# Performance work log

Hardware: AMD Instinct MI355X
Metric: run time of the kernel (lower is better)

## Reference

```python
import jax, jax.numpy as jnp
import numpy as np

ALPHA_MAX = 0.1


def setup_inputs() -> dict:
    key = jax.random.key(0)
    ks = jax.random.split(key, 9)
    B, M, L = 256, 3, 100000
    A, H = 4096, 512
    return {
        "x": jax.random.uniform(ks[0], (B, M, L), dtype=jnp.float32),  # log1p scores, non-negative
        "active_idx": jax.random.randint(ks[1], (A,), 0, L, dtype=jnp.int64 if jax.config.jax_enable_x64 else jnp.int32),
        "global_logits": jnp.log(jnp.full((M,), 1.0 / M, dtype=jnp.float32) + 1e-12),
        "delta_w": 0.01 * jax.random.normal(ks[2], (M, L), dtype=jnp.float32),
        "bias": 0.01 * jax.random.normal(ks[3], (L,), dtype=jnp.float32),
        "log_alpha": jnp.float32(-3.0),
        "hidden_w": jax.random.normal(ks[4], (H, M * A), dtype=jnp.float32) * (1.0 / np.sqrt(M * A)),
        "hidden_b": 0.01 * jax.random.normal(ks[5], (H,), dtype=jnp.float32),
        "delta_layer_w": jax.random.normal(ks[6], (A, H), dtype=jnp.float32) * (1.0 / np.sqrt(H)),
        "delta_layer_b": 0.01 * jax.random.normal(ks[7], (A,), dtype=jnp.float32),
    }


def reference(x, active_idx, global_logits, delta_w, bias, log_alpha,
              hidden_w, hidden_b, delta_layer_w, delta_layer_b):
    B = x.shape[0]
    # base logits: elementwise weighted sum over the 3 models, per-label weights
    w_eff = jax.nn.softmax(global_logits)[:, None] + delta_w          # (M, L)
    logits = jnp.einsum("bml,ml->bl", x, w_eff) + bias                # (B, L)
    # gather active labels -> 2-layer MLP (dropout is identity in eval)
    x_active = x[:, :, active_idx].reshape(B, -1)                     # (B, M*A)
    h = jax.nn.relu(x_active @ hidden_w.T + hidden_b)                 # (B, H)
    delta_active = h @ delta_layer_w.T + delta_layer_b                # (B, A)
    # scaled scatter-add back into full logits (duplicates accumulate)
    alpha = ALPHA_MAX * jax.nn.sigmoid(log_alpha)
    logits = logits.at[:, active_idx].add(alpha * delta_active)
    return logits
```

## Files before the change

kernel.cpp:

```cpp
#include <hip/hip_runtime.h>
#include <math.h>

#define B_ 256
#define M_ 3
#define L_ 100000
#define A_ 4096
#define H_ 512
#define MA_ (M_*A_)
#define K1_ MA_
#define NZ_ 16
#define KC1_ (K1_/NZ_)
#define BCHUNK_ 4

#define NWIN_    98
#define NB_LGX_  98
#define NB_LG_   (NB_LGX_*(B_/BCHUNK_))
#define NB_HW_   3072
#define NB_W2_   1024

typedef __attribute__((ext_vector_type(8))) short bf16x8;
typedef __attribute__((ext_vector_type(8))) unsigned short u16x8;
typedef __attribute__((ext_vector_type(4))) float f32x4;
typedef __attribute__((ext_vector_type(4))) int i32x4;

static __device__ __forceinline__ f32x4 ld4(const float* p) {
    return *reinterpret_cast<const f32x4*>(p);
}
static __device__ __forceinline__ f32x4 ld4nt(const float* p) {
    return __builtin_nontemporal_load(reinterpret_cast<const f32x4*>(p));
}
static __device__ __forceinline__ void st4nt(float* p, f32x4 v) {
    __builtin_nontemporal_store(v, reinterpret_cast<f32x4*>(p));
}
static __device__ __forceinline__ unsigned short f2bf(float f) {
    unsigned u = __float_as_uint(f);
    unsigned r = (u + 0x7FFFu + ((u >> 16) & 1u)) >> 16;
    return (unsigned short)r;
}

__global__ void init_head(int* __restrict__ head) {
    int i = blockIdx.x * blockDim.x + threadIdx.x;
    if (i < L_ / 4) {
        i32x4 m1 = {-1, -1, -1, -1};
        *reinterpret_cast<i32x4*>(head + i * 4) = m1;
    }
}

__global__ void window_hist(const int* __restrict__ idx, int* __restrict__ jbase) {
    __shared__ int cnt[NWIN_];
    for (int w = threadIdx.x; w < NWIN_; w += 256) cnt[w] = 0;
    __syncthreads();
    for (int a = threadIdx.x; a < A_; a += 256) atomicAdd(&cnt[idx[a] >> 10], 1);
    __syncthreads();
    if (threadIdx.x == 0) {
        int s = 0;
        for (int w = 0; w < NWIN_; ++w) { jbase[w] = s; s += cnt[w]; }
        jbase[NWIN_] = s;
    }
}

__global__ void build_perm(const int* __restrict__ idx, const int* __restrict__ jbase,
                           int* __restrict__ a_of_j, int* __restrict__ l_of_j,
                           int* __restrict__ head2) {
    __shared__ int ml[A_];
    __shared__ int ma[A_];
    __shared__ int nm_sh;
    int w = blockIdx.x, tid = threadIdx.x;
    if (tid == 0) nm_sh = 0;
    __syncthreads();
    for (int a = tid; a < A_; a += 256) {
        int l = idx[a];
        if ((l >> 10) == w) { int p = atomicAdd(&nm_sh, 1); ml[p] = l; ma[p] = a; }
    }
    __syncthreads();
    int nm = nm_sh;
    int base = jbase[w];
    for (int p = tid; p < nm; p += 256) {
        int l = ml[p], a = ma[p];
        int rank = 0, same_smaller = 0;
        for (int q = 0; q < nm; ++q) {
            int lq = ml[q], aq = ma[q];
            rank += (lq < l) | ((lq == l) & (aq < a));
            same_smaller += ((lq == l) & (aq < a));
        }
        int j = base + rank;
        a_of_j[j] = a;
        l_of_j[j] = l;
        if (same_smaller == 0) head2[l] = j;
    }
    if (w == 0 && tid == 0) l_of_j[A_] = -1;
}

__global__ __launch_bounds__(256) void mega(
    const float* __restrict__ x, const float* __restrict__ gl,
    const float* __restrict__ dw, const float* __restrict__ bias,
    const int* __restrict__ head2, const int* __restrict__ l_of_j,
    const int* __restrict__ a_of_j,
    float* __restrict__ logits, unsigned short* __restrict__ xa,
    const float* __restrict__ hw, unsigned short* __restrict__ hwb,
    const float* __restrict__ w2, unsigned short* __restrict__ w2b) {
    int bid = blockIdx.x;
    int tid = threadIdx.x;

    if (bid >= NB_LG_) {
        if (bid < NB_LG_ + NB_HW_) {
            int i = (bid - NB_LG_) * 256 + tid;
            int o = i * 8;
            int n = o / MA_;
            int col = o % MA_;
            int m = col >> 12, j0 = col & (A_ - 1);
            const float* row = hw + (size_t)n * MA_ + (m << 12);
            u16x8 out;
            #pragma unroll
            for (int t = 0; t < 8; ++t) out[t] = f2bf(row[a_of_j[j0 + t]]);
            *reinterpret_cast<u16x8*>(hwb + (size_t)o) = out;
        } else {
            int i = (bid - NB_LG_ - NB_HW_) * 256 + tid;
            f32x4 v0 = ld4nt(w2 + (size_t)i * 8);
            f32x4 v1 = ld4nt(w2 + (size_t)i * 8 + 4);
            u16x8 o;
            o[0] = f2bf(v0.x); o[1] = f2bf(v0.y); o[2] = f2bf(v0.z); o[3] = f2bf(v0.w);
            o[4] = f2bf(v1.x); o[5] = f2bf(v1.y); o[6] = f2bf(v1.z); o[7] = f2bf(v1.w);
            *reinterpret_cast<u16x8*>(w2b + (size_t)i * 8) = o;
        }
        return;
    }

    const int L4 = L_ / 4;
    int i = (bid % NB_LGX_) * 256 + tid;
    if (i >= L4) return;
    int l = i * 4;
    int b0 = (bid / NB_LGX_) * BCHUNK_;

    float g0 = gl[0], g1 = gl[1], g2 = gl[2];
    float mx = fmaxf(g0, fmaxf(g1, g2));
    float e0 = expf(g0 - mx), e1 = expf(g1 - mx), e2 = expf(g2 - mx);
    float inv = 1.0f / (e0 + e1 + e2);
    float s0 = e0 * inv, s1 = e1 * inv, s2 = e2 * inv;

    f32x4 w0 = ld4(dw + l) + s0;
    f32x4 w1 = ld4(dw + L_ + l) + s1;
    f32x4 w2v = ld4(dw + 2 * L_ + l) + s2;
    f32x4 bb = ld4(bias + l);

    i32x4 heads = *reinterpret_cast<const i32x4*>(head2 + l);

    f32x4 X[BCHUNK_][3];
    #pragma unroll
    for (int c = 0; c < BCHUNK_; ++c) {
        const float* xb = x + (size_t)(b0 + c) * M_ * L_ + l;
        X[c][0] = ld4nt(xb);
        X[c][1] = ld4nt(xb + L_);
        X[c][2] = ld4nt(xb + 2 * L_);
    }
    #pragma unroll
    for (int c = 0; c < BCHUNK_; ++c) {
        f32x4 o = X[c][0] * w0 + X[c][1] * w1 + X[c][2] * w2v + bb;
        st4nt(logits + (size_t)(b0 + c) * L_ + l, o);
    }

    #pragma unroll
    for (int c = 0; c < 4; ++c) {
        int j = heads[c];
        if (j >= 0) {
            int lh = l + c;
            do {
                #pragma unroll
                for (int b = 0; b < BCHUNK_; ++b) {
                    unsigned short* xab = xa + (size_t)(b0 + b) * MA_;
                    xab[j]          = f2bf(X[b][0][c]);
                    xab[A_ + j]     = f2bf(X[b][1][c]);
                    xab[2 * A_ + j] = f2bf(X[b][2][c]);
                }
                ++j;
            } while (l_of_j[j] == lh);
        }
    }
}

__global__ __launch_bounds__(256) void gemm1_mfma(
    const unsigned short* __restrict__ Xa, const unsigned short* __restrict__ W,
    float* __restrict__ part) {
    int tid = threadIdx.x;
    int wave = tid >> 6, lane = tid & 63;
    int row0 = blockIdx.x * 64 + (wave >> 1) * 32;
    int col0 = blockIdx.y * 64 + (wave & 1) * 32;
    int k0 = blockIdx.z * KC1_;
    int lr = lane & 15;
    int lk = (lane >> 4) * 8;
    const unsigned short* pa0 = Xa + (size_t)(row0 + lr) * K1_ + k0 + lk;
    const unsigned short* pa1 = pa0 + (size_t)16 * K1_;
    const unsigned short* pb0 = W + (size_t)(col0 + lr) * K1_ + k0 + lk;
    const unsigned short* pb1 = pb0 + (size_t)16 * K1_;
    f32x4 acc00 = {0.f,0.f,0.f,0.f}, acc01 = {0.f,0.f,0.f,0.f};
    f32x4 acc10 = {0.f,0.f,0.f,0.f}, acc11 = {0.f,0.f,0.f,0.f};
    #pragma unroll 4
    for (int k = 0; k < KC1_; k += 32) {
        bf16x8 a0 = *reinterpret_cast<const bf16x8*>(pa0 + k);
        bf16x8 a1 = *reinterpret_cast<const bf16x8*>(pa1 + k);
        bf16x8 b0 = *reinterpret_cast<const bf16x8*>(pb0 + k);
        bf16x8 b1 = *reinterpret_cast<const bf16x8*>(pb1 + k);
        acc00 = __builtin_amdgcn_mfma_f32_16x16x32_bf16(a0, b0, acc00, 0, 0, 0);
        acc01 = __builtin_amdgcn_mfma_f32_16x16x32_bf16(a0, b1, acc01, 0, 0, 0);
        acc10 = __builtin_amdgcn_mfma_f32_16x16x32_bf16(a1, b0, acc10, 0, 0, 0);
        acc11 = __builtin_amdgcn_mfma_f32_16x16x32_bf16(a1, b1, acc11, 0, 0, 0);
    }
    float* base = part + (size_t)blockIdx.z * B_ * H_;
    #pragma unroll
    for (int j = 0; j < 4; ++j) {
        int r = (lane >> 4) * 4 + j;
        base[(size_t)(row0 + r) * H_ + col0 + lr]           = acc00[j];
        base[(size_t)(row0 + r) * H_ + col0 + 16 + lr]      = acc01[j];
        base[(size_t)(row0 + 16 + r) * H_ + col0 + lr]      = acc10[j];
        base[(size_t)(row0 + 16 + r) * H_ + col0 + 16 + lr] = acc11[j];
    }
}

__global__ void reduce_relu(const float* __restrict__ part,
                            const float* __restrict__ hb,
                            unsigned short* __restrict__ h) {
    int t = blockIdx.x * blockDim.x + threadIdx.x;
    if (t >= B_ * H_) return;
    int n = t & (H_ - 1);
    float s = hb[n];
    #pragma unroll
    for (int z = 0; z < NZ_; ++z) s += part[(size_t)z * B_ * H_ + t];
    h[t] = f2bf(fmaxf(s, 0.0f));
}

__global__ __launch_bounds__(256) void gemm2_scatter(
    const unsigned short* __restrict__ Hm, const unsigned short* __restrict__ W2,
    const float* __restrict__ b2, const float* __restrict__ la,
    const int* __restrict__ idx, float* __restrict__ logits) {
    int tid = threadIdx.x;
    int wave = tid >> 6, lane = tid & 63;
    int row0 = blockIdx.x * 64 + (wave >> 1) * 32;
    int col0 = blockIdx.y * 64 + (wave & 1) * 32;
    int lr = lane & 15;
    int lk = (lane >> 4) * 8;
    const unsigned short* pa0 = Hm + (size_t)(row0 + lr) * H_ + lk;
    const unsigned short* pa1 = pa0 + (size_t)16 * H_;
    const unsigned short* pb0 = W2 + (size_t)(col0 + lr) * H_ + lk;
    const unsigned short* pb1 = pb0 + (size_t)16 * H_;
    f32x4 acc00 = {0.f,0.f,0.f,0.f}, acc01 = {0.f,0.f,0.f,0.f};
    f32x4 acc10 = {0.f,0.f,0.f,0.f}, acc11 = {0.f,0.f,0.f,0.f};
    #pragma unroll 4
    for (int k = 0; k < H_; k += 32) {
        bf16x8 a0 = *reinterpret_cast<const bf16x8*>(pa0 + k);
        bf16x8 a1 = *reinterpret_cast<const bf16x8*>(pa1 + k);
        bf16x8 b0 = *reinterpret_cast<const bf16x8*>(pb0 + k);
        bf16x8 b1 = *reinterpret_cast<const bf16x8*>(pb1 + k);
        acc00 = __builtin_amdgcn_mfma_f32_16x16x32_bf16(a0, b0, acc00, 0, 0, 0);
        acc01 = __builtin_amdgcn_mfma_f32_16x16x32_bf16(a0, b1, acc01, 0, 0, 0);
        acc10 = __builtin_amdgcn_mfma_f32_16x16x32_bf16(a1, b0, acc10, 0, 0, 0);
        acc11 = __builtin_amdgcn_mfma_f32_16x16x32_bf16(a1, b1, acc11, 0, 0, 0);
    }
    float alpha = 0.1f / (1.0f + expf(-la[0]));
    int c0 = col0 + lr, c1 = col0 + 16 + lr;
    int l0 = idx[c0], l1 = idx[c1];
    float bias0 = b2[c0], bias1 = b2[c1];
    #pragma unroll
    for (int j = 0; j < 4; ++j) {
        int r = (lane >> 4) * 4 + j;
        atomicAdd(&logits[(size_t)(row0 + r) * L_ + l0],      alpha * (acc00[j] + bias0));
        atomicAdd(&logits[(size_t)(row0 + r) * L_ + l1],      alpha * (acc01[j] + bias1));
        atomicAdd(&logits[(size_t)(row0 + 16 + r) * L_ + l0], alpha * (acc10[j] + bias0));
        atomicAdd(&logits[(size_t)(row0 + 16 + r) * L_ + l1], alpha * (acc11[j] + bias1));
    }
}

static inline size_t align256(size_t x) { return (x + 255) & ~(size_t)255; }

extern "C" void kernel_launch(void* const* d_in, const int* in_sizes, int n_in,
                              void* d_out, int out_size, void* d_ws, size_t ws_size,
                              hipStream_t stream) {
    const float* x    = (const float*)d_in[0];
    const int*   idx  = (const int*)d_in[1];
    const float* gl   = (const float*)d_in[2];
    const float* dw   = (const float*)d_in[3];
    const float* bias = (const float*)d_in[4];
    const float* la   = (const float*)d_in[5];
    const float* hw   = (const float*)d_in[6];
    const float* hb   = (const float*)d_in[7];
    const float* w2   = (const float*)d_in[8];
    const float* b2   = (const float*)d_in[9];
    float* logits = (float*)d_out;

    char* ws = (char*)d_ws;
    int* head2 = (int*)ws;                     ws += align256((size_t)L_ * 4);
    int* jbase = (int*)ws;                     ws += align256((size_t)(NWIN_ + 1) * 4);
    int* a_of_j = (int*)ws;                    ws += align256((size_t)A_ * 4);
    int* l_of_j = (int*)ws;                    ws += align256((size_t)(A_ + 1) * 4);
    unsigned short* xa = (unsigned short*)ws;  ws += align256((size_t)B_ * MA_ * 2);
    unsigned short* hwb = (unsigned short*)ws; ws += align256((size_t)H_ * MA_ * 2);
    unsigned short* w2b = (unsigned short*)ws; ws += align256((size_t)A_ * H_ * 2);
    float* part = (float*)ws;                  ws += align256((size_t)NZ_ * B_ * H_ * 4);
    unsigned short* h = (unsigned short*)ws;   ws += align256((size_t)B_ * H_ * 2);

    init_head<<<(L_ / 4 + 255) / 256, 256, 0, stream>>>(head2);
    window_hist<<<1, 256, 0, stream>>>(idx, jbase);
    build_perm<<<NWIN_, 256, 0, stream>>>(idx, jbase, a_of_j, l_of_j, head2);

    mega<<<NB_LG_ + NB_HW_ + NB_W2_, 256, 0, stream>>>(
        x, gl, dw, bias, head2, l_of_j, a_of_j, logits, xa, hw, hwb, w2, w2b);

    gemm1_mfma<<<dim3(B_ / 64, H_ / 64, NZ_), 256, 0, stream>>>(xa, hwb, part);
    reduce_relu<<<(B_ * H_ + 255) / 256, 256, 0, stream>>>(part, hb, h);
    gemm2_scatter<<<dim3(B_ / 64, A_ / 64), 256, 0, stream>>>(h, w2b, b2, la, idx, logits);
}
```

Measured before the change: 199.3 us.

## Reorder mega blocks: conversions first, one batch row and 8 labels per thread

The fused kernel now schedules the weight-conversion blocks (hidden_w gather and w2 to bf16) before the logits blocks. Each logits thread handles one batch row and 8 consecutive labels instead of 4 batch rows and 4 labels, and all loads are issued up front behind a scheduling barrier. This is meant to raise memory-level parallelism per thread and let the conversion work start early. The cost is reloading dw, bias and head2 once per batch row instead of once per 4 rows, so traffic on those arrays rises, though they are likely cache-resident.

Result: slower. 235.2 us (+18.0%).

```diff
diff --git a/kernel.cpp b/kernel.cpp
--- a/kernel.cpp
+++ b/kernel.cpp
@@ -10,13 +10,13 @@
 #define K1_ MA_
 #define NZ_ 16
 #define KC1_ (K1_/NZ_)
-#define BCHUNK_ 4
 
 #define NWIN_    98
-#define NB_LGX_  98
-#define NB_LG_   (NB_LGX_*(B_/BCHUNK_))
 #define NB_HW_   3072
 #define NB_W2_   1024
+#define NB_CVT_  (NB_HW_+NB_W2_)
+#define NB_LGX_  49
+#define NB_LG_   (NB_LGX_*B_)
 
 typedef __attribute__((ext_vector_type(8))) short bf16x8;
 typedef __attribute__((ext_vector_type(8))) unsigned short u16x8;
@@ -102,9 +102,9 @@
     int bid = blockIdx.x;
     int tid = threadIdx.x;
 
-    if (bid >= NB_LG_) {
-        if (bid < NB_LG_ + NB_HW_) {
-            int i = (bid - NB_LG_) * 256 + tid;
+    if (bid < NB_CVT_) {
+        if (bid < NB_HW_) {
+            int i = bid * 256 + tid;
             int o = i * 8;
             int n = o / MA_;
             int col = o % MA_;
@@ -115,7 +115,7 @@
             for (int t = 0; t < 8; ++t) out[t] = f2bf(row[a_of_j[j0 + t]]);
             *reinterpret_cast<u16x8*>(hwb + (size_t)o) = out;
         } else {
-            int i = (bid - NB_LG_ - NB_HW_) * 256 + tid;
+            int i = (bid - NB_HW_) * 256 + tid;
             f32x4 v0 = ld4nt(w2 + (size_t)i * 8);
             f32x4 v1 = ld4nt(w2 + (size_t)i * 8 + 4);
             u16x8 o;
@@ -126,11 +126,32 @@
         return;
     }
 
-    const int L4 = L_ / 4;
-    int i = (bid % NB_LGX_) * 256 + tid;
-    if (i >= L4) return;
-    int l = i * 4;
-    int b0 = (bid / NB_LGX_) * BCHUNK_;
+    int lgbid = bid - NB_CVT_;
+    const int L8 = L_ / 8;
+    int i = (lgbid % NB_LGX_) * 256 + tid;
+    if (i >= L8) return;
+    int l = i * 8;
+    int b = lgbid / NB_LGX_;
+
+    const float* xb = x + (size_t)b * M_ * L_ + l;
+    f32x4 X[3][2];
+    #pragma unroll
+    for (int m = 0; m < 3; ++m) {
+        X[m][0] = ld4nt(xb + (size_t)m * L_);
+        X[m][1] = ld4nt(xb + (size_t)m * L_ + 4);
+    }
+    f32x4 dwv[3][2];
+    #pragma unroll
+    for (int m = 0; m < 3; ++m) {
+        dwv[m][0] = ld4(dw + (size_t)m * L_ + l);
+        dwv[m][1] = ld4(dw + (size_t)m * L_ + l + 4);
+    }
+    f32x4 bb0 = ld4(bias + l);
+    f32x4 bb1 = ld4(bias + l + 4);
+    i32x4 h0 = *reinterpret_cast<const i32x4*>(head2 + l);
+    i32x4 h1 = *reinterpret_cast<const i32x4*>(head2 + l + 4);
+
+    __builtin_amdgcn_sched_barrier(0);
 
     float g0 = gl[0], g1 = gl[1], g2 = gl[2];
     float mx = fmaxf(g0, fmaxf(g1, g2));
@@ -138,40 +159,28 @@
     float inv = 1.0f / (e0 + e1 + e2);
     float s0 = e0 * inv, s1 = e1 * inv, s2 = e2 * inv;
 
-    f32x4 w0 = ld4(dw + l) + s0;
-    f32x4 w1 = ld4(dw + L_ + l) + s1;
-    f32x4 w2v = ld4(dw + 2 * L_ + l) + s2;
-    f32x4 bb = ld4(bias + l);
-
-    i32x4 heads = *reinterpret_cast<const i32x4*>(head2 + l);
-
-    f32x4 X[BCHUNK_][3];
-    #pragma unroll
-    for (int c = 0; c < BCHUNK_; ++c) {
-        const float* xb = x + (size_t)(b0 + c) * M_ * L_ + l;
-        X[c][0] = ld4nt(xb);
-        X[c][1] = ld4nt(xb + L_);
-        X[c][2] = ld4nt(xb + 2 * L_);
-    }
-    #pragma unroll
-    for (int c = 0; c < BCHUNK_; ++c) {
-        f32x4 o = X[c][0] * w0 + X[c][1] * w1 + X[c][2] * w2v + bb;
-        st4nt(logits + (size_t)(b0 + c) * L_ + l, o);
-    }
-
-    #pragma unroll
-    for (int c = 0; c < 4; ++c) {
+    f32x4 o0 = X[0][0] * (dwv[0][0] + s0) + X[1][0] * (dwv[1][0] + s1)
+             + X[2][0] * (dwv[2][0] + s2) + bb0;
+    f32x4 o1 = X[0][1] * (dwv[0][1] + s0) + X[1][1] * (dwv[1][1] + s1)
+             + X[2][1] * (dwv[2][1] + s2) + bb1;
+    st4nt(logits + (size_t)b * L_ + l, o0);
+    st4nt(logits + (size_t)b * L_ + l + 4, o1);
+
+    int heads[8] = {h0[0], h0[1], h0[2], h0[3], h1[0], h1[1], h1[2], h1[3]};
+    unsigned short* xab = xa + (size_t)b * MA_;
+    #pragma unroll
+    for (int c = 0; c < 8; ++c) {
         int j = heads[c];
         if (j >= 0) {
             int lh = l + c;
+            int hi = c >> 2, lo = c & 3;
+            unsigned short v0 = f2bf(X[0][hi][lo]);
+            unsigned short v1 = f2bf(X[1][hi][lo]);
+            unsigned short v2 = f2bf(X[2][hi][lo]);
             do {
-                #pragma unroll
-                for (int b = 0; b < BCHUNK_; ++b) {
-                    unsigned short* xab = xa + (size_t)(b0 + b) * MA_;
-                    xab[j]          = f2bf(X[b][0][c]);
-                    xab[A_ + j]     = f2bf(X[b][1][c]);
-                    xab[2 * A_ + j] = f2bf(X[b][2][c]);
-                }
+                xab[j]          = v0;
+                xab[A_ + j]     = v1;
+                xab[2 * A_ + j] = v2;
                 ++j;
             } while (l_of_j[j] == lh);
         }
@@ -301,7 +310,7 @@
     window_hist<<<1, 256, 0, stream>>>(idx, jbase);
     build_perm<<<NWIN_, 256, 0, stream>>>(idx, jbase, a_of_j, l_of_j, head2);
 
-    mega<<<NB_LG_ + NB_HW_ + NB_W2_, 256, 0, stream>>>(
+    mega<<<NB_CVT_ + NB_LG_, 256, 0, stream>>>(
         x, gl, dw, bias, head2, l_of_j, a_of_j, logits, xa, hw, hwb, w2, w2b);
 
     gemm1_mfma<<<dim3(B_ / 64, H_ / 64, NZ_), 256, 0, stream>>>(xa, hwb, part);
```

## Merge prepass kernels and enlarge gemm1 per-wave tile to 64x64

Applied to the files above, without the earlier changes.

Replaces the three index-preprocessing kernels (head init, window histogram, permutation build) with a single prepass. Each block clears its own slice of head2 and computes its window base offset from a shared-memory copy of the indices, which removes two launches and the jbase buffer. gemm1 is retiled so each wave computes a 64x64 output tile with 16 MFMAs per k-step instead of 32x32 with 4, giving more register-level reuse of the loaded A/B fragments. The cost is a grid that shrinks from 512 to 128 blocks and higher register pressure, which may leave CUs idle and reduce latency hiding.

Result: faster. 190.2 us (-4.6%).

```diff
diff --git a/kernel.cpp b/kernel.cpp
--- a/kernel.cpp
+++ b/kernel.cpp
@@ -38,43 +38,31 @@
     return (unsigned short)r;
 }
 
-__global__ void init_head(int* __restrict__ head) {
-    int i = blockIdx.x * blockDim.x + threadIdx.x;
-    if (i < L_ / 4) {
-        i32x4 m1 = {-1, -1, -1, -1};
-        *reinterpret_cast<i32x4*>(head + i * 4) = m1;
-    }
-}
-
-__global__ void window_hist(const int* __restrict__ idx, int* __restrict__ jbase) {
-    __shared__ int cnt[NWIN_];
-    for (int w = threadIdx.x; w < NWIN_; w += 256) cnt[w] = 0;
-    __syncthreads();
-    for (int a = threadIdx.x; a < A_; a += 256) atomicAdd(&cnt[idx[a] >> 10], 1);
-    __syncthreads();
-    if (threadIdx.x == 0) {
-        int s = 0;
-        for (int w = 0; w < NWIN_; ++w) { jbase[w] = s; s += cnt[w]; }
-        jbase[NWIN_] = s;
-    }
-}
-
-__global__ void build_perm(const int* __restrict__ idx, const int* __restrict__ jbase,
-                           int* __restrict__ a_of_j, int* __restrict__ l_of_j,
-                           int* __restrict__ head2) {
+__global__ __launch_bounds__(256) void prepass(
+    const int* __restrict__ idx, int* __restrict__ a_of_j,
+    int* __restrict__ l_of_j, int* __restrict__ head2) {
+    __shared__ int sidx[A_];
     __shared__ int ml[A_];
     __shared__ int ma[A_];
     __shared__ int nm_sh;
+    __shared__ int base_sh;
     int w = blockIdx.x, tid = threadIdx.x;
-    if (tid == 0) nm_sh = 0;
+    for (int i = tid; i < 1024; i += 256) {
+        int l = (w << 10) + i;
+        if (l < L_) head2[l] = -1;
+    }
+    for (int a = tid; a < A_; a += 256) sidx[a] = idx[a];
+    if (tid == 0) { nm_sh = 0; base_sh = 0; }
     __syncthreads();
+    int cnt_lt = 0;
     for (int a = tid; a < A_; a += 256) {
-        int l = idx[a];
-        if ((l >> 10) == w) { int p = atomicAdd(&nm_sh, 1); ml[p] = l; ma[p] = a; }
-    }
+        int wa = sidx[a] >> 10;
+        cnt_lt += (wa < w) ? 1 : 0;
+        if (wa == w) { int p = atomicAdd(&nm_sh, 1); ml[p] = sidx[a]; ma[p] = a; }
+    }
+    atomicAdd(&base_sh, cnt_lt);
     __syncthreads();
-    int nm = nm_sh;
-    int base = jbase[w];
+    int nm = nm_sh, base = base_sh;
     for (int p = tid; p < nm; p += 256) {
         int l = ml[p], a = ma[p];
         int rank = 0, same_smaller = 0;
@@ -183,36 +171,43 @@
     float* __restrict__ part) {
     int tid = threadIdx.x;
     int wave = tid >> 6, lane = tid & 63;
-    int row0 = blockIdx.x * 64 + (wave >> 1) * 32;
-    int col0 = blockIdx.y * 64 + (wave & 1) * 32;
-    int k0 = blockIdx.z * KC1_;
+    int row0 = wave * 64;
+    int col0 = blockIdx.x * 64;
+    int k0 = blockIdx.y * KC1_;
     int lr = lane & 15;
     int lk = (lane >> 4) * 8;
-    const unsigned short* pa0 = Xa + (size_t)(row0 + lr) * K1_ + k0 + lk;
-    const unsigned short* pa1 = pa0 + (size_t)16 * K1_;
-    const unsigned short* pb0 = W + (size_t)(col0 + lr) * K1_ + k0 + lk;
-    const unsigned short* pb1 = pb0 + (size_t)16 * K1_;
-    f32x4 acc00 = {0.f,0.f,0.f,0.f}, acc01 = {0.f,0.f,0.f,0.f};
-    f32x4 acc10 = {0.f,0.f,0.f,0.f}, acc11 = {0.f,0.f,0.f,0.f};
-    #pragma unroll 4
+    const unsigned short* pa[4];
+    const unsigned short* pb[4];
+    #pragma unroll
+    for (int i = 0; i < 4; ++i) {
+        pa[i] = Xa + (size_t)(row0 + i * 16 + lr) * K1_ + k0 + lk;
+        pb[i] = W + (size_t)(col0 + i * 16 + lr) * K1_ + k0 + lk;
+    }
+    f32x4 acc[4][4] = {};
+    #pragma unroll 2
     for (int k = 0; k < KC1_; k += 32) {
-        bf16x8 a0 = *reinterpret_cast<const bf16x8*>(pa0 + k);
-        bf16x8 a1 = *reinterpret_cast<const bf16x8*>(pa1 + k);
-        bf16x8 b0 = *reinterpret_cast<const bf16x8*>(pb0 + k);
-        bf16x8 b1 = *reinterpret_cast<const bf16x8*>(pb1 + k);
-        acc00 = __builtin_amdgcn_mfma_f32_16x16x32_bf16(a0, b0, acc00, 0, 0, 0);
-        acc01 = __builtin_amdgcn_mfma_f32_16x16x32_bf16(a0, b1, acc01, 0, 0, 0);
-        acc10 = __builtin_amdgcn_mfma_f32_16x16x32_bf16(a1, b0, acc10, 0, 0, 0);
-        acc11 = __builtin_amdgcn_mfma_f32_16x16x32_bf16(a1, b1, acc11, 0, 0, 0);
-    }
-    float* base = part + (size_t)blockIdx.z * B_ * H_;
-    #pragma unroll
-    for (int j = 0; j < 4; ++j) {
-        int r = (lane >> 4) * 4 + j;
-        base[(size_t)(row0 + r) * H_ + col0 + lr]           = acc00[j];
-        base[(size_t)(row0 + r) * H_ + col0 + 16 + lr]      = acc01[j];
-        base[(size_t)(row0 + 16 + r) * H_ + col0 + lr]      = acc10[j];
-        base[(size_t)(row0 + 16 + r) * H_ + col0 + 16 + lr] = acc11[j];
+        bf16x8 av[4], bv[4];
+        #pragma unroll
+        for (int i = 0; i < 4; ++i) av[i] = *reinterpret_cast<const bf16x8*>(pa[i] + k);
+        #pragma unroll
+        for (int i = 0; i < 4; ++i) bv[i] = *reinterpret_cast<const bf16x8*>(pb[i] + k);
+        #pragma unroll
+        for (int i = 0; i < 4; ++i)
+            #pragma unroll
+            for (int j = 0; j < 4; ++j)
+                acc[i][j] = __builtin_amdgcn_mfma_f32_16x16x32_bf16(av[i], bv[j], acc[i][j], 0, 0, 0);
+    }
+    float* base = part + (size_t)blockIdx.y * B_ * H_;
+    #pragma unroll
+    for (int i = 0; i < 4; ++i) {
+        #pragma unroll
+        for (int j = 0; j < 4; ++j) {
+            #pragma unroll
+            for (int r = 0; r < 4; ++r) {
+                int rr = (lane >> 4) * 4 + r;
+                base[(size_t)(row0 + i * 16 + rr) * H_ + col0 + j * 16 + lr] = acc[i][j][r];
+            }
+        }
     }
 }
 
@@ -288,7 +283,6 @@
 
     char* ws = (char*)d_ws;
     int* head2 = (int*)ws;                     ws += align256((size_t)L_ * 4);
-    int* jbase = (int*)ws;                     ws += align256((size_t)(NWIN_ + 1) * 4);
     int* a_of_j = (int*)ws;                    ws += align256((size_t)A_ * 4);
     int* l_of_j = (int*)ws;                    ws += align256((size_t)(A_ + 1) * 4);
     unsigned short* xa = (unsigned short*)ws;  ws += align256((size_t)B_ * MA_ * 2);
@@ -297,14 +291,12 @@
     float* part = (float*)ws;                  ws += align256((size_t)NZ_ * B_ * H_ * 4);
     unsigned short* h = (unsigned short*)ws;   ws += align256((size_t)B_ * H_ * 2);
 
-    init_head<<<(L_ / 4 + 255) / 256, 256, 0, stream>>>(head2);
-    window_hist<<<1, 256, 0, stream>>>(idx, jbase);
-    build_perm<<<NWIN_, 256, 0, stream>>>(idx, jbase, a_of_j, l_of_j, head2);
+    prepass<<<NWIN_, 256, 0, stream>>>(idx, a_of_j, l_of_j, head2);
 
     mega<<<NB_LG_ + NB_HW_ + NB_W2_, 256, 0, stream>>>(
         x, gl, dw, bias, head2, l_of_j, a_of_j, logits, xa, hw, hwb, w2, w2b);
 
-    gemm1_mfma<<<dim3(B_ / 64, H_ / 64, NZ_), 256, 0, stream>>>(xa, hwb, part);
+    gemm1_mfma<<<dim3(H_ / 64, NZ_), 256, 0, stream>>>(xa, hwb, part);
     reduce_relu<<<(B_ * H_ + 255) / 256, 256, 0, stream>>>(part, hb, h);
     gemm2_scatter<<<dim3(B_ / 64, A_ / 64), 256, 0, stream>>>(h, w2b, b2, la, idx, logits);
 }
```
